# Optimization experiments

Measured on AMD Instinct MI355X. Metric: run time of the kernel, lower is better.

Reference implementation:

```python
import jax, jax.numpy as jnp
import numpy as np

N, E, F, ED = 50000, 400000, 64, 32
K = 5            # ceil(0.0001 * N) for the single graph (batch is all zeros)
EPS = 1e-5


def setup_inputs():
    key = jax.random.key(0)
    def p(i, shape, s=0.05):
        return jax.random.normal(jax.random.fold_in(key, i), shape, jnp.float32) * s
    return {
        "x": jax.random.normal(jax.random.fold_in(key, 100), (N, F), jnp.float32),
        "edge_index": jax.random.randint(jax.random.fold_in(key, 101), (2, E), 0, N),
        "edge_attr": jax.random.normal(jax.random.fold_in(key, 102), (E, ED), jnp.float32),
        "batch": jnp.zeros((N,), jnp.int32),
        # PNAConv layer 1: towers=1, F_in=F, F_out=F
        "We1": p(0, (ED, F)), "be1": p(1, (F,)),
        "preW1": p(2, (1, 3 * F, F)), "preb1": p(3, (1, F)),
        "postW1": p(4, (1, 13 * F, F)), "postb1": p(5, (1, F)),
        "linW1": p(6, (F, F)), "linb1": p(7, (F,)),
        "bn1_g": jnp.ones((F,), jnp.float32), "bn1_b": jnp.zeros((F,), jnp.float32),
        # PNAConv layer 2: towers=4, F_in=F (divide_input=False), F_out=F//4
        "We2": p(8, (ED, F)), "be2": p(9, (F,)),
        "preW2": p(10, (4, 3 * F, F)), "preb2": p(11, (4, F)),
        "postW2": p(12, (4, 13 * F, F // 4)), "postb2": p(13, (4, F // 4)),
        "linW2": p(14, (F, F)), "linb2": p(15, (F,)),
        "bn2_g": jnp.ones((F,), jnp.float32), "bn2_b": jnp.zeros((F,), jnp.float32),
        # SAGPooling scorer: GraphConv(F -> 1)
        "poolWrel": p(16, (F, 1)), "poolbrel": p(17, (1,)),
        "poolWroot": p(18, (F, 1)),
        # final MLP 64 -> 32 -> 16 -> 2
        "mW1": p(19, (F, F // 2)), "mb1": p(20, (F // 2,)),
        "mW2": p(21, (F // 2, F // 4)), "mb2": p(22, (F // 4,)),
        "mW3": p(23, (F // 4, 2)), "mb3": p(24, (2,)),
    }


def _pna_conv(x, row, col, e, We, be, preW, preb, postW, postb, linW, linb, avg_log):
    Nn, Fi = x.shape
    T = preW.shape[0]
    deg = jax.ops.segment_sum(jnp.ones(row.shape[0], x.dtype), col, num_segments=Nn)
    d = jnp.maximum(deg, 1.0)
    e_enc = e @ We + be                              # [E, Fi]
    x_i, x_j = x[col], x[row]                        # [E, Fi]
    Wi, Wj, Wee = preW[:, :Fi], preW[:, Fi:2 * Fi], preW[:, 2 * Fi:]
    # per-tower pre-MLP on concat([x_i, x_j, e_enc]) without materializing the concat
    h = (jnp.einsum('ef,tfg->etg', x_i, Wi)
         + jnp.einsum('ef,tfg->etg', x_j, Wj)
         + jnp.einsum('ef,tfg->etg', e_enc, Wee)
         + preb[None])                               # [E, T, Fi]
    dn = d[:, None, None]
    mean = jax.ops.segment_sum(h, col, num_segments=Nn) / dn
    mean2 = jax.ops.segment_sum(h * h, col, num_segments=Nn) / dn
    std = jnp.sqrt(jax.nn.relu(mean2 - mean * mean) + EPS)
    has = (deg > 0)[:, None, None]
    mn = jnp.where(has, jax.ops.segment_min(h, col, num_segments=Nn), 0.0)
    mx = jnp.where(has, jax.ops.segment_max(h, col, num_segments=Nn), 0.0)
    agg = jnp.concatenate([mean, mn, mx, std], axis=-1)           # [N, T, 4Fi]
    amp = (jnp.log(d + 1.0) / avg_log)[:, None, None]
    att = (avg_log / jnp.log(d + 1.0))[:, None, None]
    scaled = jnp.concatenate([agg, agg * amp, agg * att], axis=-1)  # [N, T, 12Fi]
    xt = jnp.broadcast_to(x[:, None, :], (Nn, T, Fi))
    out = jnp.concatenate([xt, scaled], axis=-1)                   # [N, T, 13Fi]
    out = jnp.einsum('ntf,tfg->ntg', out, postW) + postb[None]     # [N, T, F_out]
    out = out.reshape(Nn, -1)
    return out @ linW + linb


def _bn_relu(x, g, b):
    m = x.mean(0)
    v = ((x - m) ** 2).mean(0)
    return jax.nn.relu((x - m) / jnp.sqrt(v + EPS) * g + b)


def reference(x, edge_index, edge_attr, batch,
              We1, be1, preW1, preb1, postW1, postb1, linW1, linb1, bn1_g, bn1_b,
              We2, be2, preW2, preb2, postW2, postb2, linW2, linb2, bn2_g, bn2_b,
              poolWrel, poolbrel, poolWroot,
              mW1, mb1, mW2, mb2, mW3, mb3):
    row, col = edge_index[0], edge_index[1]
    deg = jax.ops.segment_sum(jnp.ones(E, jnp.float32), col, num_segments=N)
    avg_log = jnp.mean(jnp.log(deg + 1.0))   # PNA avg_deg['log'] from degree histogram
    h = _bn_relu(_pna_conv(x, row, col, edge_attr, We1, be1, preW1, preb1, postW1, postb1, linW1, linb1, avg_log), bn1_g, bn1_b)
    h = _bn_relu(_pna_conv(h, row, col, edge_attr, We2, be2, preW2, preb2, postW2, postb2, linW2, linb2, avg_log), bn2_g, bn2_b)
    # SAGPooling: GraphConv score, topk (single graph), gated gather
    nsum = jax.ops.segment_sum(h[row], col, num_segments=N)
    score = (nsum @ poolWrel + poolbrel + h @ poolWroot).reshape(-1)
    topv, perm = jax.lax.top_k(score, K)
    xp = h[perm] * jnp.tanh(topv)[:, None]
    z = jax.nn.relu(xp @ mW1 + mb1)
    z = jax.nn.relu(z @ mW2 + mb2)
    return z @ mW3 + mb3
```

## Files before the change

kernel.cpp:

```cpp
#include <hip/hip_runtime.h>
#include <math.h>
#include <limits.h>

#define NN 50000
#define NE 400000
#define FD 64
#define EDD 32
#define EPSF 1e-5f


__global__ void k_deg(const int* __restrict__ ei, int* __restrict__ cnt) {
    int e = blockIdx.x * 256 + threadIdx.x;
    if (e < NE) atomicAdd(&cnt[ei[NE + e]], 1);
}

__global__ void k_avglog(const int* __restrict__ cnt, float* __restrict__ scal) {
    int n = blockIdx.x * 256 + threadIdx.x;
    float v = 0.f;
    if (n < NN) v = logf((float)cnt[n] + 1.0f);
    for (int o = 32; o >= 1; o >>= 1) v += __shfl_xor(v, o);
    if ((threadIdx.x & 63) == 0) atomicAdd(&scal[0], v);
}

__global__ __launch_bounds__(256) void k_scan1(const int* __restrict__ cnt,
                                               int* __restrict__ part, int* __restrict__ bsum) {
    __shared__ int buf[256];
    int i = blockIdx.x * 256 + threadIdx.x;
    int v = (i < NN) ? cnt[i] : 0;
    buf[threadIdx.x] = v;
    __syncthreads();
    for (int s = 1; s < 256; s <<= 1) {
        int t = (threadIdx.x >= (unsigned)s) ? buf[threadIdx.x - s] : 0;
        __syncthreads();
        buf[threadIdx.x] += t;
        __syncthreads();
    }
    if (i < NN) part[i] = buf[threadIdx.x] - v;
    if (threadIdx.x == 255) bsum[blockIdx.x] = buf[255];
}

__global__ __launch_bounds__(256) void k_scan2(const int* __restrict__ bsum,
                                               int* __restrict__ boff,
                                               float* __restrict__ scal, int nb) {
    __shared__ int buf[256];
    int tid = threadIdx.x;
    int v = (tid < nb) ? bsum[tid] : 0;
    buf[tid] = v;
    __syncthreads();
    for (int s = 1; s < 256; s <<= 1) {
        int t = (tid >= s) ? buf[tid - s] : 0;
        __syncthreads();
        buf[tid] += t;
        __syncthreads();
    }
    boff[tid] = buf[tid] - v;
    if (tid == nb - 1) boff[nb] = buf[tid];
    if (tid == 0) scal[1] = scal[0] / (float)NN;
}

__global__ void k_scan3(const int* __restrict__ part, const int* __restrict__ boff,
                        int* __restrict__ offv, int* __restrict__ cnt) {
    int i = blockIdx.x * 256 + threadIdx.x;
    if (i < NN) {
        offv[i] = part[i] + boff[blockIdx.x];
        cnt[i] = 0;
    }
    if (i == 0) offv[NN] = boff[gridDim.x];
}

__global__ void k_scatter(const int* __restrict__ ei, const int* __restrict__ offv,
                          int* __restrict__ cnt, int2* __restrict__ spair) {
    int e = blockIdx.x * 256 + threadIdx.x;
    if (e < NE) {
        int n = ei[NE + e];
        int p = offv[n] + atomicAdd(&cnt[n], 1);
        spair[p] = make_int2(ei[e], e);
    }
}

__global__ void k_ampatt(const int* __restrict__ offv, const float* __restrict__ scal,
                         float* __restrict__ ampv, float* __restrict__ attv) {
    int n = blockIdx.x * 256 + threadIdx.x;
    if (n >= NN) return;
    float degf = (float)(offv[n + 1] - offv[n]);
    float d = fmaxf(degf, 1.f);
    float lg = logf(d + 1.f);
    float al = scal[1];
    ampv[n] = lg / al;
    attv[n] = al / lg;
}


__global__ void k_weff(const float* __restrict__ We, const float* __restrict__ be,
                       const float* __restrict__ preW, float* __restrict__ weff) {
    int idx = blockIdx.x * 256 + threadIdx.x;
    if (idx >= 33 * 64) return;
    int k = idx >> 6, g = idx & 63;
    const float* Wee = preW + 128 * 64;
    float acc = 0.f;
    if (k < EDD) {
        for (int f = 0; f < FD; ++f) acc += We[k * FD + f] * Wee[f * FD + g];
    } else {
        for (int f = 0; f < FD; ++f) acc += be[f] * Wee[f * FD + g];
    }
    weff[idx] = acc;
}

__global__ __launch_bounds__(256) void k_uc(const float* __restrict__ xin,
                                            const float* __restrict__ preW,
                                            const float* __restrict__ preb,
                                            const float* __restrict__ weff,
                                            float* __restrict__ u, float* __restrict__ cvec) {
    int g = threadIdx.x & 63;
    int nsub = threadIdx.x >> 6;
    float wU[FD], wC[FD];
#pragma unroll
    for (int f = 0; f < FD; ++f) {
        wC[f] = preW[f * 64 + g];
        wU[f] = preW[(64 + f) * 64 + g];
    }
    float cb = preb[g] + weff[32 * 64 + g];
    __shared__ float xs[4 * 72];
    for (int base = blockIdx.x * 4; base < NN; base += gridDim.x * 4) {
        __syncthreads();
        {
            int i = threadIdx.x;
            int node = base + (i >> 6);
            xs[(i >> 6) * 72 + (i & 63)] = (node < NN) ? xin[(size_t)node * 64 + (i & 63)] : 0.f;
        }
        __syncthreads();
        int n = base + nsub;
        if (n < NN) {
            const float* xv = &xs[nsub * 72];
            float aU = 0.f, aC = 0.f;
#pragma unroll
            for (int f = 0; f < FD; ++f) {
                float x = xv[f];
                aU += x * wU[f];
                aC += x * wC[f];
            }
            u[(size_t)n * 64 + g] = aU;
            cvec[(size_t)n * 64 + g] = aC + cb;
        }
    }
}

__global__ __launch_bounds__(256) void k_edge(const float* __restrict__ eattr,
                                              const int* __restrict__ offv,
                                              const int2* __restrict__ spair,
                                              const float* __restrict__ u,
                                              const float* __restrict__ cvec,
                                              const float* __restrict__ weff,
                                              float* __restrict__ agg) {
    int wv = threadIdx.x >> 6, lane = threadIdx.x & 63;
    int n = blockIdx.x * 4 + wv;
    float wreg[32];
#pragma unroll
    for (int k = 0; k < 32; ++k) wreg[k] = weff[k * 64 + lane];
    int p0 = offv[n], p1 = offv[n + 1];
    float sm = 0.f, sq = 0.f, mn = INFINITY, mx = -INFINITY;
    int p = p0;
    for (; p + 1 < p1; p += 2) {
        int2 se0 = spair[p];
        int2 se1 = spair[p + 1];
        int src0 = __builtin_amdgcn_readfirstlane(se0.x);
        int eid0 = __builtin_amdgcn_readfirstlane(se0.y);
        int src1 = __builtin_amdgcn_readfirstlane(se1.x);
        int eid1 = __builtin_amdgcn_readfirstlane(se1.y);
        const float* __restrict__ ea0 = eattr + (size_t)eid0 * EDD;
        const float* __restrict__ ea1 = eattr + (size_t)eid1 * EDD;
        float v0 = u[(size_t)src0 * 64 + lane];
        float v1 = u[(size_t)src1 * 64 + lane];
#pragma unroll
        for (int k = 0; k < 32; ++k) {
            v0 += ea0[k] * wreg[k];
            v1 += ea1[k] * wreg[k];
        }
        sm += v0;
        sq += v0 * v0;
        mn = fminf(mn, v0);
        mx = fmaxf(mx, v0);
        sm += v1;
        sq += v1 * v1;
        mn = fminf(mn, v1);
        mx = fmaxf(mx, v1);
    }
    if (p < p1) {
        int2 se = spair[p];
        int src = __builtin_amdgcn_readfirstlane(se.x);
        int eid = __builtin_amdgcn_readfirstlane(se.y);
        const float* __restrict__ ea = eattr + (size_t)eid * EDD;
        float v = u[(size_t)src * 64 + lane];
#pragma unroll
        for (int k = 0; k < 32; ++k) v += ea[k] * wreg[k];
        sm += v;
        sq += v * v;
        mn = fminf(mn, v);
        mx = fmaxf(mx, v);
    }
    float degf = (float)(p1 - p0);
    float d = fmaxf(degf, 1.f);
    float c = cvec[(size_t)n * 64 + lane];
    float sh = sm + degf * c;
    float mean = sh / d;
    float m2 = (sq + 2.f * c * sm + degf * c * c) / d;
    float var = fmaxf(m2 - mean * mean, 0.f);
    float sd = sqrtf(var + EPSF);
    float mnv = (degf > 0.f) ? mn + c : 0.f;
    float mxv = (degf > 0.f) ? mx + c : 0.f;
    size_t b = (size_t)n * 256 + lane;
    agg[b] = mean;
    agg[b + 64] = mnv;
    agg[b + 128] = mxv;
    agg[b + 192] = sd;
}

template <int PNPT>
__global__ __launch_bounds__(256) void k_postF(const float* __restrict__ xin,
                                               const float* __restrict__ agg,
                                               const float* __restrict__ ampv,
                                               const float* __restrict__ attv,
                                               const float* __restrict__ P,
                                               int pstride,
                                               const float* __restrict__ pbias,
                                               float* __restrict__ tgb, int cb) {
    __shared__ __align__(16) float wsh[832 * 16];
    int tid = threadIdx.x;
    int sc = blockIdx.x * 16;
    for (int i = tid; i < 832 * 4; i += 256) {
        int row = i >> 2, c4 = (i & 3) * 4;
        *(float4*)&wsh[row * 16 + c4] = *(const float4*)&P[(size_t)row * pstride + sc + c4];
    }
    __syncthreads();
    int cidx = (tid & 3) * 4;
    int grp = tid >> 2;
    int nb = blockIdx.y * (64 * PNPT) + grp * PNPT;
    int nd[PNPT];
    float amp[PNPT], att[PNPT];
#pragma unroll
    for (int k = 0; k < PNPT; ++k) {
        nd[k] = (nb + k < NN) ? nb + k : NN - 1;
        amp[k] = ampv[nd[k]];
        att[k] = attv[nd[k]];
    }
    float accA[PNPT][4], accB[PNPT][4], accC[PNPT][4];
#pragma unroll
    for (int k = 0; k < PNPT; ++k)
#pragma unroll
        for (int c = 0; c < 4; ++c) { accA[k][c] = 0.f; accB[k][c] = 0.f; accC[k][c] = 0.f; }
#pragma unroll 4
    for (int q = 0; q < 64; q += 4) {
        float4 w[4];
#pragma unroll
        for (int r = 0; r < 4; ++r) w[r] = *(const float4*)&wsh[(q + r) * 16 + cidx];
#pragma unroll
        for (int k = 0; k < PNPT; ++k) {
            float4 xv = *(const float4*)&xin[(size_t)nd[k] * 64 + q];
            float xa[4] = {xv.x, xv.y, xv.z, xv.w};
#pragma unroll
            for (int r = 0; r < 4; ++r) {
                accA[k][0] += xa[r] * w[r].x;
                accA[k][1] += xa[r] * w[r].y;
                accA[k][2] += xa[r] * w[r].z;
                accA[k][3] += xa[r] * w[r].w;
            }
        }
    }
#pragma unroll 2
    for (int q = 0; q < 256; q += 4) {
        float4 w1[4], w2[4], w3[4];
#pragma unroll
        for (int r = 0; r < 4; ++r) {
            w1[r] = *(const float4*)&wsh[(64 + q + r) * 16 + cidx];
            w2[r] = *(const float4*)&wsh[(320 + q + r) * 16 + cidx];
            w3[r] = *(const float4*)&wsh[(576 + q + r) * 16 + cidx];
        }
#pragma unroll
        for (int k = 0; k < PNPT; ++k) {
            float4 av = *(const float4*)&agg[(size_t)nd[k] * 256 + q];
            float aa[4] = {av.x, av.y, av.z, av.w};
#pragma unroll
            for (int r = 0; r < 4; ++r) {
                accA[k][0] += aa[r] * w1[r].x;
                accA[k][1] += aa[r] * w1[r].y;
                accA[k][2] += aa[r] * w1[r].z;
                accA[k][3] += aa[r] * w1[r].w;
                accB[k][0] += aa[r] * w2[r].x;
                accB[k][1] += aa[r] * w2[r].y;
                accB[k][2] += aa[r] * w2[r].z;
                accB[k][3] += aa[r] * w2[r].w;
                accC[k][0] += aa[r] * w3[r].x;
                accC[k][1] += aa[r] * w3[r].y;
                accC[k][2] += aa[r] * w3[r].z;
                accC[k][3] += aa[r] * w3[r].w;
            }
        }
    }
    float4 pbv = *(const float4*)&pbias[sc + cidx];
    float pb[4] = {pbv.x, pbv.y, pbv.z, pbv.w};
#pragma unroll
    for (int k = 0; k < PNPT; ++k) {
        int node = nb + k;
        if (node < NN) {
            float4 o;
            o.x = pb[0] + accA[k][0] + amp[k] * accB[k][0] + att[k] * accC[k][0];
            o.y = pb[1] + accA[k][1] + amp[k] * accB[k][1] + att[k] * accC[k][1];
            o.z = pb[2] + accA[k][2] + amp[k] * accB[k][2] + att[k] * accC[k][2];
            o.w = pb[3] + accA[k][3] + amp[k] * accB[k][3] + att[k] * accC[k][3];
            *(float4*)&tgb[(size_t)node * 64 + cb + sc + cidx] = o;
        }
    }
}

__global__ __launch_bounds__(256) void k_lin(const float* __restrict__ tgb,
                                             const float* __restrict__ linW,
                                             const float* __restrict__ linb,
                                             float* __restrict__ pre, float* __restrict__ bn) {
    __shared__ float ts[4 * 72];
    __shared__ float rs[256], rs2[256];
    int c = threadIdx.x & 63, r = threadIdx.x >> 6;
    float w[64];
#pragma unroll
    for (int f = 0; f < 64; ++f) w[f] = linW[f * 64 + c];
    float lb = linb[c];
    float s = 0.f, s2 = 0.f;
    for (int base = blockIdx.x * 4; base < NN; base += gridDim.x * 4) {
        __syncthreads();
        {
            int i = threadIdx.x;
            int node = base + (i >> 6);
            ts[(i >> 6) * 72 + (i & 63)] = (node < NN) ? tgb[(size_t)node * 64 + (i & 63)] : 0.f;
        }
        __syncthreads();
        int n = base + r;
        if (n < NN) {
            const float* tv = &ts[r * 72];
            float a = lb;
#pragma unroll
            for (int f = 0; f < 64; ++f) a += tv[f] * w[f];
            pre[(size_t)n * 64 + c] = a;
            s += a;
            s2 += a * a;
        }
    }
    __syncthreads();
    rs[threadIdx.x] = s;
    rs2[threadIdx.x] = s2;
    __syncthreads();
    if (threadIdx.x < 64) {
        float S = rs[c] + rs[c + 64] + rs[c + 128] + rs[c + 192];
        float S2 = rs2[c] + rs2[c + 64] + rs2[c + 128] + rs2[c + 192];
        atomicAdd(&bn[c], S);
        atomicAdd(&bn[64 + c], S2);
    }
}

__global__ void k_bnrelu(const float* __restrict__ pre, const float* __restrict__ bn,
                         const float* __restrict__ gg, const float* __restrict__ bb,
                         float* __restrict__ h) {
    int i = blockIdx.x * 256 + threadIdx.x;
    if (i >= NN * 64) return;
    int c = i & 63;
    float m = bn[c] * (1.f / (float)NN);
    float v = bn[64 + c] * (1.f / (float)NN) - m * m;
    float x = (pre[i] - m) / sqrtf(v + EPSF) * gg[c] + bb[c];
    h[i] = fmaxf(x, 0.f);
}


__global__ void k_pooldots(const float* __restrict__ h, const float* __restrict__ wrel,
                           const float* __restrict__ wroot, float* __restrict__ s1,
                           float* __restrict__ s2) {
    int wv = threadIdx.x >> 6, lane = threadIdx.x & 63;
    int n = blockIdx.x * 4 + wv;
    if (n >= NN) return;
    float x = h[(size_t)n * 64 + lane];
    float d1 = x * wrel[lane];
    float d2 = x * wroot[lane];
    for (int o = 32; o >= 1; o >>= 1) {
        d1 += __shfl_xor(d1, o);
        d2 += __shfl_xor(d2, o);
    }
    if (lane == 0) { s1[n] = d1; s2[n] = d2; }
}

__global__ void k_score(const float* __restrict__ s1, const float* __restrict__ s2,
                        const int* __restrict__ offv, const int2* __restrict__ spair,
                        const float* __restrict__ pb, float* __restrict__ score) {
    int n = blockIdx.x * 256 + threadIdx.x;
    if (n >= NN) return;
    float sc = pb[0] + s2[n];
    int p1 = offv[n + 1];
    for (int p = offv[n]; p < p1; ++p) sc += s1[spair[p].x];
    score[n] = sc;
}

#define TOPB 64
#define TOPCHUNK 782

__global__ __launch_bounds__(256) void k_top1(const float* __restrict__ score,
                                              float* __restrict__ candv, int* __restrict__ candi) {
    __shared__ float bs[256];
    __shared__ int bi[256];
    __shared__ int chosen[5];
    int b = blockIdx.x;
    int start = b * TOPCHUNK;
    int end = start + TOPCHUNK;
    if (end > NN) end = NN;
    for (int r = 0; r < 5; ++r) {
        float best = -INFINITY;
        int bidx = -1;
        for (int i = start + (int)threadIdx.x; i < end; i += 256) {
            bool skip = false;
            for (int q = 0; q < r; ++q)
                if (chosen[q] == i) skip = true;
            if (!skip) {
                float sv = score[i];
                if (sv > best || (sv == best && (bidx == -1 || i < bidx))) { best = sv; bidx = i; }
            }
        }
        bs[threadIdx.x] = best;
        bi[threadIdx.x] = bidx;
        __syncthreads();
        for (int s = 128; s >= 1; s >>= 1) {
            if ((int)threadIdx.x < s) {
                float s2v = bs[threadIdx.x + s];
                int i2 = bi[threadIdx.x + s];
                float s1v = bs[threadIdx.x];
                int i1 = bi[threadIdx.x];
                if (i2 != -1 && (s2v > s1v || (s2v == s1v && (i1 == -1 || i2 < i1)))) {
                    bs[threadIdx.x] = s2v;
                    bi[threadIdx.x] = i2;
                }
            }
            __syncthreads();
        }
        if (threadIdx.x == 0) {
            candv[b * 5 + r] = bs[0];
            candi[b * 5 + r] = bi[0];
            chosen[r] = bi[0];
        }
        __syncthreads();
    }
}

__global__ __launch_bounds__(320) void k_top2(const float* __restrict__ candv,
                                              const int* __restrict__ candi,
                                              float* __restrict__ topv, int* __restrict__ topi) {
    __shared__ float bs[320];
    __shared__ int bi[320];
    __shared__ int used[320];
    __shared__ float wbest[5];
    __shared__ int wnode[5], wpos[5];
    int tid = threadIdx.x;
    bs[tid] = candv[tid];
    bi[tid] = candi[tid];
    used[tid] = (bi[tid] == -1) ? 1 : 0;
    __syncthreads();
    int wv = tid >> 6, lane = tid & 63;
    for (int r = 0; r < 5; ++r) {
        float s = used[tid] ? -INFINITY : bs[tid];
        int nd = used[tid] ? INT_MAX : bi[tid];
        int pos = tid;
        for (int o = 32; o >= 1; o >>= 1) {
            float s2 = __shfl_xor(s, o);
            int nd2 = __shfl_xor(nd, o);
            int p2 = __shfl_xor(pos, o);
            if (s2 > s || (s2 == s && nd2 < nd)) { s = s2; nd = nd2; pos = p2; }
        }
        if (lane == 0) { wbest[wv] = s; wnode[wv] = nd; wpos[wv] = pos; }
        __syncthreads();
        if (tid == 0) {
            float best = wbest[0];
            int bnode = wnode[0], bpos = wpos[0];
            for (int i = 1; i < 5; ++i)
                if (wbest[i] > best || (wbest[i] == best && wnode[i] < bnode)) {
                    best = wbest[i];
                    bnode = wnode[i];
                    bpos = wpos[i];
                }
            used[bpos] = 1;
            topv[r] = best;
            topi[r] = bnode;
        }
        __syncthreads();
    }
}

__global__ __launch_bounds__(320) void k_mlp(const float* __restrict__ h,
                                             const float* __restrict__ topv,
                                             const int* __restrict__ topi,
                                             const float* __restrict__ mW1, const float* __restrict__ mb1,
                                             const float* __restrict__ mW2, const float* __restrict__ mb2,
                                             const float* __restrict__ mW3, const float* __restrict__ mb3,
                                             float* __restrict__ out) {
    __shared__ float xp[5 * 64], z1[5 * 32], z2[5 * 16];
    int tid = threadIdx.x;
    int k = tid >> 6, f = tid & 63;
    xp[k * 64 + f] = h[(size_t)topi[k] * 64 + f] * tanhf(topv[k]);
    __syncthreads();
    if (tid < 5 * 32) {
        int kk = tid >> 5, j = tid & 31;
        float a = mb1[j];
        for (int f2 = 0; f2 < 64; ++f2) a += xp[kk * 64 + f2] * mW1[f2 * 32 + j];
        z1[tid] = fmaxf(a, 0.f);
    }
    __syncthreads();
    if (tid < 5 * 16) {
        int kk = tid >> 4, j = tid & 15;
        float a = mb2[j];
        for (int f2 = 0; f2 < 32; ++f2) a += z1[kk * 32 + f2] * mW2[f2 * 16 + j];
        z2[tid] = fmaxf(a, 0.f);
    }
    __syncthreads();
    if (tid < 10) {
        int kk = tid >> 1, j = tid & 1;
        float a = mb3[j];
        for (int f2 = 0; f2 < 16; ++f2) a += z2[kk * 16 + f2] * mW3[f2 * 2 + j];
        out[tid] = a;
    }
}


extern "C" void kernel_launch(void* const* d_in, const int* in_sizes, int n_in,
                              void* d_out, int out_size, void* d_ws, size_t ws_size,
                              hipStream_t stream) {
    const float* x = (const float*)d_in[0];
    const int* ei = (const int*)d_in[1];
    const float* eattr = (const float*)d_in[2];
    const float* We1 = (const float*)d_in[4];
    const float* be1 = (const float*)d_in[5];
    const float* preW1 = (const float*)d_in[6];
    const float* preb1 = (const float*)d_in[7];
    const float* postW1 = (const float*)d_in[8];
    const float* postb1 = (const float*)d_in[9];
    const float* linW1 = (const float*)d_in[10];
    const float* linb1 = (const float*)d_in[11];
    const float* bn1g = (const float*)d_in[12];
    const float* bn1b = (const float*)d_in[13];
    const float* We2 = (const float*)d_in[14];
    const float* be2 = (const float*)d_in[15];
    const float* preW2 = (const float*)d_in[16];
    const float* preb2 = (const float*)d_in[17];
    const float* postW2 = (const float*)d_in[18];
    const float* postb2 = (const float*)d_in[19];
    const float* linW2 = (const float*)d_in[20];
    const float* linb2 = (const float*)d_in[21];
    const float* bn2g = (const float*)d_in[22];
    const float* bn2b = (const float*)d_in[23];
    const float* wrel = (const float*)d_in[24];
    const float* pbrel = (const float*)d_in[25];
    const float* wroot = (const float*)d_in[26];
    const float* mW1 = (const float*)d_in[27];
    const float* mb1 = (const float*)d_in[28];
    const float* mW2 = (const float*)d_in[29];
    const float* mb2 = (const float*)d_in[30];
    const float* mW3 = (const float*)d_in[31];
    const float* mb3 = (const float*)d_in[32];
    float* out = (float*)d_out;

    char* w = (char*)d_ws;
    size_t o = 0;
    auto alloc = [&](size_t bytes) {
        size_t r = o;
        o = (o + bytes + 255) & ~(size_t)255;
        return r;
    };
    int* cnt = (int*)(w + alloc((size_t)NN * 4));
    int* offv = (int*)(w + alloc((size_t)(NN + 1) * 4));
    int2* spair = (int2*)(w + alloc((size_t)NE * 8));
    int* part = (int*)(w + alloc((size_t)NN * 4));
    int* bsum = (int*)(w + alloc(256 * 4));
    int* boff = (int*)(w + alloc(260 * 4));
    float* scal = (float*)(w + alloc(64 * 4));
    float* bnst = (float*)(w + alloc(128 * 4));
    float* weff = (float*)(w + alloc((size_t)33 * 64 * 4));
    float* ampv = (float*)(w + alloc((size_t)NN * 4));
    float* attv = (float*)(w + alloc((size_t)NN * 4));
    float* u = (float*)(w + alloc((size_t)NN * 64 * 4));
    float* cvec = (float*)(w + alloc((size_t)NN * 64 * 4));
    float* agg = (float*)(w + alloc((size_t)NN * 256 * 4));
    float* tgb = (float*)(w + alloc((size_t)NN * 64 * 4));
    float* pre = (float*)(w + alloc((size_t)NN * 64 * 4));
    float* h1 = (float*)(w + alloc((size_t)NN * 64 * 4));
    float* h2 = (float*)(w + alloc((size_t)NN * 64 * 4));
    float* s1 = (float*)(w + alloc((size_t)NN * 4));
    float* s2 = (float*)(w + alloc((size_t)NN * 4));
    float* score = (float*)(w + alloc((size_t)NN * 4));
    float* candv = (float*)(w + alloc(320 * 4));
    int* candi = (int*)(w + alloc(320 * 4));
    float* topv = (float*)(w + alloc(16 * 4));
    int* topi = (int*)(w + alloc(16 * 4));
    (void)ws_size; (void)n_in; (void)in_sizes; (void)out_size;

    hipMemsetAsync(cnt, 0, (size_t)NN * 4, stream);
    hipMemsetAsync(scal, 0, 64 * 4, stream);

    int nscan = (NN + 255) / 256;

    k_deg<<<(NE + 255) / 256, 256, 0, stream>>>(ei, cnt);
    k_avglog<<<(NN + 255) / 256, 256, 0, stream>>>(cnt, scal);
    k_scan1<<<nscan, 256, 0, stream>>>(cnt, part, bsum);
    k_scan2<<<1, 256, 0, stream>>>(bsum, boff, scal, nscan);
    k_scan3<<<nscan, 256, 0, stream>>>(part, boff, offv, cnt);
    k_scatter<<<(NE + 255) / 256, 256, 0, stream>>>(ei, offv, cnt, spair);
    k_ampatt<<<(NN + 255) / 256, 256, 0, stream>>>(offv, scal, ampv, attv);

    k_weff<<<(33 * 64 + 255) / 256, 256, 0, stream>>>(We1, be1, preW1, weff);
    k_uc<<<500, 256, 0, stream>>>(x, preW1, preb1, weff, u, cvec);
    k_edge<<<NN / 4, 256, 0, stream>>>(eattr, offv, spair, u, cvec, weff, agg);
    {
        int t1 = (NN + 256 - 1) / 256;
        k_postF<4><<<dim3(4, t1), 256, 0, stream>>>(x, agg, ampv, attv, postW1, 64,
                                                    postb1, tgb, 0);
    }
    hipMemsetAsync(bnst, 0, 128 * 4, stream);
    k_lin<<<256, 256, 0, stream>>>(tgb, linW1, linb1, pre, bnst);
    k_bnrelu<<<(NN * 64) / 256, 256, 0, stream>>>(pre, bnst, bn1g, bn1b, h1);

    int t2 = (NN + 128 - 1) / 128;
    for (int t = 0; t < 4; ++t) {
        const float* pW = preW2 + (size_t)t * 192 * 64;
        const float* pP = postW2 + (size_t)t * 832 * 16;
        k_weff<<<(33 * 64 + 255) / 256, 256, 0, stream>>>(We2, be2, pW, weff);
        k_uc<<<500, 256, 0, stream>>>(h1, pW, preb2 + t * 64, weff, u, cvec);
        k_edge<<<NN / 4, 256, 0, stream>>>(eattr, offv, spair, u, cvec, weff, agg);
        k_postF<2><<<dim3(1, t2), 256, 0, stream>>>(h1, agg, ampv, attv, pP, 16,
                                                    postb2 + t * 16, tgb, t * 16);
    }
    hipMemsetAsync(bnst, 0, 128 * 4, stream);
    k_lin<<<256, 256, 0, stream>>>(tgb, linW2, linb2, pre, bnst);
    k_bnrelu<<<(NN * 64) / 256, 256, 0, stream>>>(pre, bnst, bn2g, bn2b, h2);

    k_pooldots<<<NN / 4, 256, 0, stream>>>(h2, wrel, wroot, s1, s2);
    k_score<<<(NN + 255) / 256, 256, 0, stream>>>(s1, s2, offv, spair, pbrel, score);
    k_top1<<<TOPB, 256, 0, stream>>>(score, candv, candi);
    k_top2<<<1, 320, 0, stream>>>(candv, candi, topv, topi);
    k_mlp<<<1, 320, 0, stream>>>(h2, topv, topi, mW1, mb1, mW2, mb2, mW3, mb3, out);
}
```

Before: 1.001 ms.

## Replace layer-1 post-MLP kernel with node-tiled kernel exploiting scaler factorization

Adds k_postZ for the layer-1 post-MLP. Each block stages 32 nodes' input features and aggregates in shared memory, reads weights straight from global memory, and accumulates three partial products over the aggregates: identity, amplification and attenuation. The scalers are applied once per node at the end, so the scaled aggregate copies are never multiplied separately. The kernel covers all 64 output columns per block, replacing the old 4-column-block postF layout that re-read the node data for each column slice. The cost is global weight reads per block, which rely on cache, and higher register pressure from 24 accumulators per thread.

```diff
diff --git a/kernel.cpp b/kernel.cpp
--- a/kernel.cpp
+++ b/kernel.cpp
@@ -213,6 +213,111 @@
     agg[b + 64] = mnv;
     agg[b + 128] = mxv;
     agg[b + 192] = sd;
+}
+
+#define ZSTR 324
+
+__global__ __launch_bounds__(256) void k_postZ(const float* __restrict__ xin,
+                                               const float* __restrict__ agg,
+                                               const float* __restrict__ ampv,
+                                               const float* __restrict__ attv,
+                                               const float* __restrict__ P,
+                                               const float* __restrict__ pbias,
+                                               float* __restrict__ tgb) {
+    __shared__ __align__(16) float zsh[32 * ZSTR];
+    __shared__ float ampS[32], attS[32];
+    int tid = threadIdx.x;
+    int n0 = blockIdx.x * 32;
+    for (int i = tid; i < 32 * 64; i += 256) {
+        int nd = i >> 6, col = i & 63;
+        int node = n0 + nd;
+        zsh[nd * ZSTR + col] = (node < NN) ? xin[(size_t)node * 64 + col] : 0.f;
+    }
+    for (int i = tid; i < 32 * 256; i += 256) {
+        int nd = i >> 8, col = i & 255;
+        int node = n0 + nd;
+        zsh[nd * ZSTR + 64 + col] = (node < NN) ? agg[(size_t)node * 256 + col] : 0.f;
+    }
+    if (tid < 32) {
+        int node = n0 + tid;
+        ampS[tid] = (node < NN) ? ampv[node] : 1.f;
+        attS[tid] = (node < NN) ? attv[node] : 1.f;
+    }
+    __syncthreads();
+    int cidx = (tid & 15) * 4;
+    int ng = tid >> 4;
+    float accA[2][4], accB[2][4], accC[2][4];
+#pragma unroll
+    for (int k = 0; k < 2; ++k)
+#pragma unroll
+        for (int c = 0; c < 4; ++c) { accA[k][c] = 0.f; accB[k][c] = 0.f; accC[k][c] = 0.f; }
+    const float* P0 = P;
+    const float* P1 = P + 64 * 64;
+    const float* P2 = P + 320 * 64;
+    const float* P3 = P + 576 * 64;
+#pragma unroll 4
+    for (int q = 0; q < 64; q += 4) {
+        float4 w[4];
+#pragma unroll
+        for (int r = 0; r < 4; ++r) w[r] = *(const float4*)&P0[(size_t)(q + r) * 64 + cidx];
+#pragma unroll
+        for (int k = 0; k < 2; ++k) {
+            float4 zv = *(const float4*)&zsh[(ng * 2 + k) * ZSTR + q];
+            float za[4] = {zv.x, zv.y, zv.z, zv.w};
+#pragma unroll
+            for (int r = 0; r < 4; ++r) {
+                accA[k][0] += za[r] * w[r].x;
+                accA[k][1] += za[r] * w[r].y;
+                accA[k][2] += za[r] * w[r].z;
+                accA[k][3] += za[r] * w[r].w;
+            }
+        }
+    }
+#pragma unroll 2
+    for (int q = 0; q < 256; q += 4) {
+        float4 w1[4], w2[4], w3[4];
+#pragma unroll
+        for (int r = 0; r < 4; ++r) {
+            w1[r] = *(const float4*)&P1[(size_t)(q + r) * 64 + cidx];
+            w2[r] = *(const float4*)&P2[(size_t)(q + r) * 64 + cidx];
+            w3[r] = *(const float4*)&P3[(size_t)(q + r) * 64 + cidx];
+        }
+#pragma unroll
+        for (int k = 0; k < 2; ++k) {
+            float4 av = *(const float4*)&zsh[(ng * 2 + k) * ZSTR + 64 + q];
+            float aa[4] = {av.x, av.y, av.z, av.w};
+#pragma unroll
+            for (int r = 0; r < 4; ++r) {
+                accA[k][0] += aa[r] * w1[r].x;
+                accA[k][1] += aa[r] * w1[r].y;
+                accA[k][2] += aa[r] * w1[r].z;
+                accA[k][3] += aa[r] * w1[r].w;
+                accB[k][0] += aa[r] * w2[r].x;
+                accB[k][1] += aa[r] * w2[r].y;
+                accB[k][2] += aa[r] * w2[r].z;
+                accB[k][3] += aa[r] * w2[r].w;
+                accC[k][0] += aa[r] * w3[r].x;
+                accC[k][1] += aa[r] * w3[r].y;
+                accC[k][2] += aa[r] * w3[r].z;
+                accC[k][3] += aa[r] * w3[r].w;
+            }
+        }
+    }
+    float4 pbv = *(const float4*)&pbias[cidx];
+    float pb[4] = {pbv.x, pbv.y, pbv.z, pbv.w};
+#pragma unroll
+    for (int k = 0; k < 2; ++k) {
+        int ln = ng * 2 + k;
+        int node = n0 + ln;
+        if (node < NN) {
+            float4 o;
+            o.x = pb[0] + accA[k][0] + ampS[ln] * accB[k][0] + attS[ln] * accC[k][0];
+            o.y = pb[1] + accA[k][1] + ampS[ln] * accB[k][1] + attS[ln] * accC[k][1];
+            o.z = pb[2] + accA[k][2] + ampS[ln] * accB[k][2] + attS[ln] * accC[k][2];
+            o.w = pb[3] + accA[k][3] + ampS[ln] * accB[k][3] + attS[ln] * accC[k][3];
+            *(float4*)&tgb[(size_t)node * 64 + cidx] = o;
+        }
+    }
 }
 
 template <int PNPT>
@@ -609,11 +714,7 @@
     k_weff<<<(33 * 64 + 255) / 256, 256, 0, stream>>>(We1, be1, preW1, weff);
     k_uc<<<500, 256, 0, stream>>>(x, preW1, preb1, weff, u, cvec);
     k_edge<<<NN / 4, 256, 0, stream>>>(eattr, offv, spair, u, cvec, weff, agg);
-    {
-        int t1 = (NN + 256 - 1) / 256;
-        k_postF<4><<<dim3(4, t1), 256, 0, stream>>>(x, agg, ampv, attv, postW1, 64,
-                                                    postb1, tgb, 0);
-    }
+    k_postZ<<<(NN + 31) / 32, 256, 0, stream>>>(x, agg, ampv, attv, postW1, postb1, tgb);
     hipMemsetAsync(bnst, 0, 128 * 4, stream);
     k_lin<<<256, 256, 0, stream>>>(tgb, linW1, linb1, pre, bnst);
     k_bnrelu<<<(NN * 64) / 256, 256, 0, stream>>>(pre, bnst, bn1g, bn1b, h1);
```

Result: slower. 1.106 ms (+10.5%).

## Split edge message computation from per-node aggregation to balance load

Applied to the files above, without the earlier changes.

The fused per-node edge kernel becomes two kernels. The first computes per-edge messages over a flat grid-stride loop across all edges and writes them to a new E x 64 buffer. The second reduces those messages per destination node into mean, min, max and std. This removes the per-node degree imbalance in the compute-heavy edge loop, at the cost of writing and re-reading about 100 MB of intermediate data per call, repeated five times.

```diff
diff --git a/kernel.cpp b/kernel.cpp
--- a/kernel.cpp
+++ b/kernel.cpp
@@ -145,22 +145,18 @@
     }
 }
 
-__global__ __launch_bounds__(256) void k_edge(const float* __restrict__ eattr,
-                                              const int* __restrict__ offv,
-                                              const int2* __restrict__ spair,
-                                              const float* __restrict__ u,
-                                              const float* __restrict__ cvec,
-                                              const float* __restrict__ weff,
-                                              float* __restrict__ agg) {
-    int wv = threadIdx.x >> 6, lane = threadIdx.x & 63;
-    int n = blockIdx.x * 4 + wv;
+__global__ __launch_bounds__(256) void k_edgev(const float* __restrict__ eattr,
+                                               const int2* __restrict__ spair,
+                                               const float* __restrict__ u,
+                                               const float* __restrict__ weff,
+                                               float* __restrict__ ve) {
+    int lane = threadIdx.x & 63;
+    int wid = blockIdx.x * 4 + (threadIdx.x >> 6);
+    int nw = gridDim.x * 4;
     float wreg[32];
 #pragma unroll
     for (int k = 0; k < 32; ++k) wreg[k] = weff[k * 64 + lane];
-    int p0 = offv[n], p1 = offv[n + 1];
-    float sm = 0.f, sq = 0.f, mn = INFINITY, mx = -INFINITY;
-    int p = p0;
-    for (; p + 1 < p1; p += 2) {
+    for (int p = wid * 2; p < NE; p += nw * 2) {
         int2 se0 = spair[p];
         int2 se1 = spair[p + 1];
         int src0 = __builtin_amdgcn_readfirstlane(se0.x);
@@ -176,27 +172,33 @@
             v0 += ea0[k] * wreg[k];
             v1 += ea1[k] * wreg[k];
         }
-        sm += v0;
-        sq += v0 * v0;
-        mn = fminf(mn, v0);
-        mx = fmaxf(mx, v0);
-        sm += v1;
-        sq += v1 * v1;
-        mn = fminf(mn, v1);
-        mx = fmaxf(mx, v1);
-    }
-    if (p < p1) {
-        int2 se = spair[p];
-        int src = __builtin_amdgcn_readfirstlane(se.x);
-        int eid = __builtin_amdgcn_readfirstlane(se.y);
-        const float* __restrict__ ea = eattr + (size_t)eid * EDD;
-        float v = u[(size_t)src * 64 + lane];
-#pragma unroll
-        for (int k = 0; k < 32; ++k) v += ea[k] * wreg[k];
-        sm += v;
-        sq += v * v;
-        mn = fminf(mn, v);
-        mx = fmaxf(mx, v);
+        ve[(size_t)p * 64 + lane] = v0;
+        ve[(size_t)(p + 1) * 64 + lane] = v1;
+    }
+}
+
+__global__ __launch_bounds__(256) void k_stats(const int* __restrict__ offv,
+                                               const float* __restrict__ ve,
+                                               const float* __restrict__ cvec,
+                                               float* __restrict__ agg) {
+    int wv = threadIdx.x >> 6, lane = threadIdx.x & 63;
+    int n = blockIdx.x * 4 + wv;
+    int p0 = offv[n], p1 = offv[n + 1];
+    float sm = 0.f, sq = 0.f, mn = INFINITY, mx = -INFINITY;
+    int p = p0;
+    for (; p + 3 < p1; p += 4) {
+        float v0 = ve[(size_t)p * 64 + lane];
+        float v1 = ve[(size_t)(p + 1) * 64 + lane];
+        float v2 = ve[(size_t)(p + 2) * 64 + lane];
+        float v3 = ve[(size_t)(p + 3) * 64 + lane];
+        sm += v0; sq += v0 * v0; mn = fminf(mn, v0); mx = fmaxf(mx, v0);
+        sm += v1; sq += v1 * v1; mn = fminf(mn, v1); mx = fmaxf(mx, v1);
+        sm += v2; sq += v2 * v2; mn = fminf(mn, v2); mx = fmaxf(mx, v2);
+        sm += v3; sq += v3 * v3; mn = fminf(mn, v3); mx = fmaxf(mx, v3);
+    }
+    for (; p < p1; ++p) {
+        float v = ve[(size_t)p * 64 + lane];
+        sm += v; sq += v * v; mn = fminf(mn, v); mx = fmaxf(mx, v);
     }
     float degf = (float)(p1 - p0);
     float d = fmaxf(degf, 1.f);
@@ -580,6 +582,7 @@
     float* u = (float*)(w + alloc((size_t)NN * 64 * 4));
     float* cvec = (float*)(w + alloc((size_t)NN * 64 * 4));
     float* agg = (float*)(w + alloc((size_t)NN * 256 * 4));
+    float* ve = (float*)(w + alloc((size_t)NE * 64 * 4));
     float* tgb = (float*)(w + alloc((size_t)NN * 64 * 4));
     float* pre = (float*)(w + alloc((size_t)NN * 64 * 4));
     float* h1 = (float*)(w + alloc((size_t)NN * 64 * 4));
@@ -608,7 +611,8 @@
 
     k_weff<<<(33 * 64 + 255) / 256, 256, 0, stream>>>(We1, be1, preW1, weff);
     k_uc<<<500, 256, 0, stream>>>(x, preW1, preb1, weff, u, cvec);
-    k_edge<<<NN / 4, 256, 0, stream>>>(eattr, offv, spair, u, cvec, weff, agg);
+    k_edgev<<<2048, 256, 0, stream>>>(eattr, spair, u, weff, ve);
+    k_stats<<<NN / 4, 256, 0, stream>>>(offv, ve, cvec, agg);
     {
         int t1 = (NN + 256 - 1) / 256;
         k_postF<4><<<dim3(4, t1), 256, 0, stream>>>(x, agg, ampv, attv, postW1, 64,
@@ -624,7 +628,8 @@
         const float* pP = postW2 + (size_t)t * 832 * 16;
         k_weff<<<(33 * 64 + 255) / 256, 256, 0, stream>>>(We2, be2, pW, weff);
         k_uc<<<500, 256, 0, stream>>>(h1, pW, preb2 + t * 64, weff, u, cvec);
-        k_edge<<<NN / 4, 256, 0, stream>>>(eattr, offv, spair, u, cvec, weff, agg);
+        k_edgev<<<2048, 256, 0, stream>>>(eattr, spair, u, weff, ve);
+        k_stats<<<NN / 4, 256, 0, stream>>>(offv, ve, cvec, agg);
         k_postF<2><<<dim3(1, t2), 256, 0, stream>>>(h1, agg, ampv, attv, pP, 16,
                                                     postb2 + t * 16, tgb, t * 16);
     }
```

After: 1.142 ms. +14.1%, slower.

## Process two PNA towers per pass in layer-2 edge and node kernels

Applied to the files above, without the earlier changes.

Layer 2's four towers used to run as four separate weff/uc/edge/postF sequences. They now run as two passes of two towers each. The edge kernel gathers the CSR neighbour lists and edge attributes once per pair of towers and computes both towers' messages from those loads, so edge traffic and launch count are roughly halved. In exchange, register use per thread rises (64 weight registers plus doubled accumulators), which may lower occupancy, and the u, cvec and agg buffers grow to twice their size.

```diff
diff --git a/kernel.cpp b/kernel.cpp
--- a/kernel.cpp
+++ b/kernel.cpp
@@ -92,7 +92,8 @@
 
 
 __global__ void k_weff(const float* __restrict__ We, const float* __restrict__ be,
-                       const float* __restrict__ preW, float* __restrict__ weff) {
+                       const float* __restrict__ preW, float* __restrict__ weff,
+                       int tf, int toff) {
     int idx = blockIdx.x * 256 + threadIdx.x;
     if (idx >= 33 * 64) return;
     int k = idx >> 6, g = idx & 63;
@@ -103,28 +104,32 @@
     } else {
         for (int f = 0; f < FD; ++f) acc += be[f] * Wee[f * FD + g];
     }
-    weff[idx] = acc;
-}
-
+    weff[k * tf + toff + g] = acc;
+}
+
+template <int T>
 __global__ __launch_bounds__(256) void k_uc(const float* __restrict__ xin,
                                             const float* __restrict__ preW,
                                             const float* __restrict__ preb,
                                             const float* __restrict__ weff,
                                             float* __restrict__ u, float* __restrict__ cvec) {
-    int g = threadIdx.x & 63;
-    int nsub = threadIdx.x >> 6;
+    constexpr int TF = 64 * T;
+    constexpr int NS = 256 / TF;
+    int col = threadIdx.x % TF;
+    int nsub = threadIdx.x / TF;
+    int t = col >> 6, g = col & 63;
+    const float* pw = preW + (size_t)t * 192 * 64;
     float wU[FD], wC[FD];
 #pragma unroll
     for (int f = 0; f < FD; ++f) {
-        wC[f] = preW[f * 64 + g];
-        wU[f] = preW[(64 + f) * 64 + g];
-    }
-    float cb = preb[g] + weff[32 * 64 + g];
-    __shared__ float xs[4 * 72];
-    for (int base = blockIdx.x * 4; base < NN; base += gridDim.x * 4) {
-        __syncthreads();
-        {
-            int i = threadIdx.x;
+        wC[f] = pw[f * 64 + g];
+        wU[f] = pw[(64 + f) * 64 + g];
+    }
+    float cb = preb[t * 64 + g] + weff[32 * TF + col];
+    __shared__ float xs[NS * 72];
+    for (int base = blockIdx.x * NS; base < NN; base += gridDim.x * NS) {
+        __syncthreads();
+        for (int i = threadIdx.x; i < NS * 64; i += 256) {
             int node = base + (i >> 6);
             xs[(i >> 6) * 72 + (i & 63)] = (node < NN) ? xin[(size_t)node * 64 + (i & 63)] : 0.f;
         }
@@ -139,12 +144,13 @@
                 aU += x * wU[f];
                 aC += x * wC[f];
             }
-            u[(size_t)n * 64 + g] = aU;
-            cvec[(size_t)n * 64 + g] = aC + cb;
-        }
-    }
-}
-
+            u[(size_t)n * TF + col] = aU;
+            cvec[(size_t)n * TF + col] = aC + cb;
+        }
+    }
+}
+
+template <int T>
 __global__ __launch_bounds__(256) void k_edge(const float* __restrict__ eattr,
                                               const int* __restrict__ offv,
                                               const int2* __restrict__ spair,
@@ -152,13 +158,18 @@
                                               const float* __restrict__ cvec,
                                               const float* __restrict__ weff,
                                               float* __restrict__ agg) {
+    constexpr int TF = 64 * T;
     int wv = threadIdx.x >> 6, lane = threadIdx.x & 63;
     int n = blockIdx.x * 4 + wv;
-    float wreg[32];
-#pragma unroll
-    for (int k = 0; k < 32; ++k) wreg[k] = weff[k * 64 + lane];
+    float wreg[32][T];
+#pragma unroll
+    for (int k = 0; k < 32; ++k)
+#pragma unroll
+        for (int t = 0; t < T; ++t) wreg[k][t] = weff[k * TF + t * 64 + lane];
     int p0 = offv[n], p1 = offv[n + 1];
-    float sm = 0.f, sq = 0.f, mn = INFINITY, mx = -INFINITY;
+    float sm[T], sq[T], mn[T], mx[T];
+#pragma unroll
+    for (int t = 0; t < T; ++t) { sm[t] = 0.f; sq[t] = 0.f; mn[t] = INFINITY; mx[t] = -INFINITY; }
     int p = p0;
     for (; p + 1 < p1; p += 2) {
         int2 se0 = spair[p];
@@ -169,67 +180,88 @@
         int eid1 = __builtin_amdgcn_readfirstlane(se1.y);
         const float* __restrict__ ea0 = eattr + (size_t)eid0 * EDD;
         const float* __restrict__ ea1 = eattr + (size_t)eid1 * EDD;
-        float v0 = u[(size_t)src0 * 64 + lane];
-        float v1 = u[(size_t)src1 * 64 + lane];
+        float v0[T], v1[T];
+#pragma unroll
+        for (int t = 0; t < T; ++t) {
+            v0[t] = u[(size_t)src0 * TF + t * 64 + lane];
+            v1[t] = u[(size_t)src1 * TF + t * 64 + lane];
+        }
 #pragma unroll
         for (int k = 0; k < 32; ++k) {
-            v0 += ea0[k] * wreg[k];
-            v1 += ea1[k] * wreg[k];
-        }
-        sm += v0;
-        sq += v0 * v0;
-        mn = fminf(mn, v0);
-        mx = fmaxf(mx, v0);
-        sm += v1;
-        sq += v1 * v1;
-        mn = fminf(mn, v1);
-        mx = fmaxf(mx, v1);
+            float a0 = ea0[k], a1 = ea1[k];
+#pragma unroll
+            for (int t = 0; t < T; ++t) {
+                v0[t] += a0 * wreg[k][t];
+                v1[t] += a1 * wreg[k][t];
+            }
+        }
+#pragma unroll
+        for (int t = 0; t < T; ++t) {
+            sm[t] += v0[t]; sq[t] += v0[t] * v0[t];
+            mn[t] = fminf(mn[t], v0[t]); mx[t] = fmaxf(mx[t], v0[t]);
+            sm[t] += v1[t]; sq[t] += v1[t] * v1[t];
+            mn[t] = fminf(mn[t], v1[t]); mx[t] = fmaxf(mx[t], v1[t]);
+        }
     }
     if (p < p1) {
         int2 se = spair[p];
         int src = __builtin_amdgcn_readfirstlane(se.x);
         int eid = __builtin_amdgcn_readfirstlane(se.y);
         const float* __restrict__ ea = eattr + (size_t)eid * EDD;
-        float v = u[(size_t)src * 64 + lane];
-#pragma unroll
-        for (int k = 0; k < 32; ++k) v += ea[k] * wreg[k];
-        sm += v;
-        sq += v * v;
-        mn = fminf(mn, v);
-        mx = fmaxf(mx, v);
+        float v[T];
+#pragma unroll
+        for (int t = 0; t < T; ++t) v[t] = u[(size_t)src * TF + t * 64 + lane];
+#pragma unroll
+        for (int k = 0; k < 32; ++k) {
+            float a = ea[k];
+#pragma unroll
+            for (int t = 0; t < T; ++t) v[t] += a * wreg[k][t];
+        }
+#pragma unroll
+        for (int t = 0; t < T; ++t) {
+            sm[t] += v[t]; sq[t] += v[t] * v[t];
+            mn[t] = fminf(mn[t], v[t]); mx[t] = fmaxf(mx[t], v[t]);
+        }
     }
     float degf = (float)(p1 - p0);
     float d = fmaxf(degf, 1.f);
-    float c = cvec[(size_t)n * 64 + lane];
-    float sh = sm + degf * c;
-    float mean = sh / d;
-    float m2 = (sq + 2.f * c * sm + degf * c * c) / d;
-    float var = fmaxf(m2 - mean * mean, 0.f);
-    float sd = sqrtf(var + EPSF);
-    float mnv = (degf > 0.f) ? mn + c : 0.f;
-    float mxv = (degf > 0.f) ? mx + c : 0.f;
-    size_t b = (size_t)n * 256 + lane;
-    agg[b] = mean;
-    agg[b + 64] = mnv;
-    agg[b + 128] = mxv;
-    agg[b + 192] = sd;
+#pragma unroll
+    for (int t = 0; t < T; ++t) {
+        float c = cvec[(size_t)n * TF + t * 64 + lane];
+        float sh = sm[t] + degf * c;
+        float mean = sh / d;
+        float m2 = (sq[t] + 2.f * c * sm[t] + degf * c * c) / d;
+        float var = fmaxf(m2 - mean * mean, 0.f);
+        float sd = sqrtf(var + EPSF);
+        float mnv = (degf > 0.f) ? mn[t] + c : 0.f;
+        float mxv = (degf > 0.f) ? mx[t] + c : 0.f;
+        size_t b = (size_t)n * (256 * T) + t * 256 + lane;
+        agg[b] = mean;
+        agg[b + 64] = mnv;
+        agg[b + 128] = mxv;
+        agg[b + 192] = sd;
+    }
 }
 
 template <int PNPT>
 __global__ __launch_bounds__(256) void k_postF(const float* __restrict__ xin,
                                                const float* __restrict__ agg,
+                                               int aggstride, int aggxoff,
                                                const float* __restrict__ ampv,
                                                const float* __restrict__ attv,
                                                const float* __restrict__ P,
-                                               int pstride,
+                                               int pxoff, int pstride,
                                                const float* __restrict__ pbias,
                                                float* __restrict__ tgb, int cb) {
     __shared__ __align__(16) float wsh[832 * 16];
     int tid = threadIdx.x;
-    int sc = blockIdx.x * 16;
+    const float* Pe = P + (size_t)blockIdx.x * pxoff;
+    const float* pbe = pbias + blockIdx.x * 16;
+    const float* agge = agg + (size_t)blockIdx.x * aggxoff;
+    int cbe = cb + blockIdx.x * 16;
     for (int i = tid; i < 832 * 4; i += 256) {
         int row = i >> 2, c4 = (i & 3) * 4;
-        *(float4*)&wsh[row * 16 + c4] = *(const float4*)&P[(size_t)row * pstride + sc + c4];
+        *(float4*)&wsh[row * 16 + c4] = *(const float4*)&Pe[(size_t)row * pstride + c4];
     }
     __syncthreads();
     int cidx = (tid & 3) * 4;
@@ -277,7 +309,7 @@
         }
 #pragma unroll
         for (int k = 0; k < PNPT; ++k) {
-            float4 av = *(const float4*)&agg[(size_t)nd[k] * 256 + q];
+            float4 av = *(const float4*)&agge[(size_t)nd[k] * aggstride + q];
             float aa[4] = {av.x, av.y, av.z, av.w};
 #pragma unroll
             for (int r = 0; r < 4; ++r) {
@@ -296,7 +328,7 @@
             }
         }
     }
-    float4 pbv = *(const float4*)&pbias[sc + cidx];
+    float4 pbv = *(const float4*)&pbe[cidx];
     float pb[4] = {pbv.x, pbv.y, pbv.z, pbv.w};
 #pragma unroll
     for (int k = 0; k < PNPT; ++k) {
@@ -307,7 +339,7 @@
             o.y = pb[1] + accA[k][1] + amp[k] * accB[k][1] + att[k] * accC[k][1];
             o.z = pb[2] + accA[k][2] + amp[k] * accB[k][2] + att[k] * accC[k][2];
             o.w = pb[3] + accA[k][3] + amp[k] * accB[k][3] + att[k] * accC[k][3];
-            *(float4*)&tgb[(size_t)node * 64 + cb + sc + cidx] = o;
+            *(float4*)&tgb[(size_t)node * 64 + cbe + cidx] = o;
         }
     }
 }
@@ -574,12 +606,12 @@
     int* boff = (int*)(w + alloc(260 * 4));
     float* scal = (float*)(w + alloc(64 * 4));
     float* bnst = (float*)(w + alloc(128 * 4));
-    float* weff = (float*)(w + alloc((size_t)33 * 64 * 4));
+    float* weff = (float*)(w + alloc((size_t)33 * 128 * 4));
     float* ampv = (float*)(w + alloc((size_t)NN * 4));
     float* attv = (float*)(w + alloc((size_t)NN * 4));
-    float* u = (float*)(w + alloc((size_t)NN * 64 * 4));
-    float* cvec = (float*)(w + alloc((size_t)NN * 64 * 4));
-    float* agg = (float*)(w + alloc((size_t)NN * 256 * 4));
+    float* u = (float*)(w + alloc((size_t)NN * 128 * 4));
+    float* cvec = (float*)(w + alloc((size_t)NN * 128 * 4));
+    float* agg = (float*)(w + alloc((size_t)NN * 512 * 4));
     float* tgb = (float*)(w + alloc((size_t)NN * 64 * 4));
     float* pre = (float*)(w + alloc((size_t)NN * 64 * 4));
     float* h1 = (float*)(w + alloc((size_t)NN * 64 * 4));
@@ -606,27 +638,31 @@
     k_scatter<<<(NE + 255) / 256, 256, 0, stream>>>(ei, offv, cnt, spair);
     k_ampatt<<<(NN + 255) / 256, 256, 0, stream>>>(offv, scal, ampv, attv);
 
-    k_weff<<<(33 * 64 + 255) / 256, 256, 0, stream>>>(We1, be1, preW1, weff);
-    k_uc<<<500, 256, 0, stream>>>(x, preW1, preb1, weff, u, cvec);
-    k_edge<<<NN / 4, 256, 0, stream>>>(eattr, offv, spair, u, cvec, weff, agg);
+    k_weff<<<(33 * 64 + 255) / 256, 256, 0, stream>>>(We1, be1, preW1, weff, 64, 0);
+    k_uc<1><<<500, 256, 0, stream>>>(x, preW1, preb1, weff, u, cvec);
+    k_edge<1><<<NN / 4, 256, 0, stream>>>(eattr, offv, spair, u, cvec, weff, agg);
     {
-        int t1 = (NN + 256 - 1) / 256;
-        k_postF<4><<<dim3(4, t1), 256, 0, stream>>>(x, agg, ampv, attv, postW1, 64,
-                                                    postb1, tgb, 0);
+        int t1 = (NN + 255) / 256;
+        k_postF<4><<<dim3(4, t1), 256, 0, stream>>>(x, agg, 256, 0, ampv, attv,
+                                                    postW1, 16, 64, postb1, tgb, 0);
     }
     hipMemsetAsync(bnst, 0, 128 * 4, stream);
     k_lin<<<256, 256, 0, stream>>>(tgb, linW1, linb1, pre, bnst);
     k_bnrelu<<<(NN * 64) / 256, 256, 0, stream>>>(pre, bnst, bn1g, bn1b, h1);
 
-    int t2 = (NN + 128 - 1) / 128;
-    for (int t = 0; t < 4; ++t) {
-        const float* pW = preW2 + (size_t)t * 192 * 64;
-        const float* pP = postW2 + (size_t)t * 832 * 16;
-        k_weff<<<(33 * 64 + 255) / 256, 256, 0, stream>>>(We2, be2, pW, weff);
-        k_uc<<<500, 256, 0, stream>>>(h1, pW, preb2 + t * 64, weff, u, cvec);
-        k_edge<<<NN / 4, 256, 0, stream>>>(eattr, offv, spair, u, cvec, weff, agg);
-        k_postF<2><<<dim3(1, t2), 256, 0, stream>>>(h1, agg, ampv, attv, pP, 16,
-                                                    postb2 + t * 16, tgb, t * 16);
+    int t2 = (NN + 127) / 128;
+    for (int pr = 0; pr < 2; ++pr) {
+        int t0 = pr * 2;
+        const float* pW0 = preW2 + (size_t)t0 * 192 * 64;
+        const float* pW1t = preW2 + (size_t)(t0 + 1) * 192 * 64;
+        k_weff<<<(33 * 64 + 255) / 256, 256, 0, stream>>>(We2, be2, pW0, weff, 128, 0);
+        k_weff<<<(33 * 64 + 255) / 256, 256, 0, stream>>>(We2, be2, pW1t, weff, 128, 64);
+        k_uc<2><<<500, 256, 0, stream>>>(h1, pW0, preb2 + t0 * 64, weff, u, cvec);
+        k_edge<2><<<NN / 4, 256, 0, stream>>>(eattr, offv, spair, u, cvec, weff, agg);
+        k_postF<2><<<dim3(2, t2), 256, 0, stream>>>(h1, agg, 512, 256, ampv, attv,
+                                                    postW2 + (size_t)t0 * 832 * 16,
+                                                    832 * 16, 16,
+                                                    postb2 + t0 * 16, tgb, t0 * 16);
     }
     hipMemsetAsync(bnst, 0, 128 * 4, stream);
     k_lin<<<256, 256, 0, stream>>>(tgb, linW2, linb2, pre, bnst);
```

Result: slower. 1.042 ms (+4.2%).
